# Kernel tuning notes

Hardware: AMD Instinct MI355X
Metric: run time of the kernel (lower is better)

## Reference

```python
import jax, jax.numpy as jnp
import numpy as np

N_EMBD = 2048
EPS = 1e-5

def layernorm(x, g, b):
    mu = jnp.mean(x, axis=-1, keepdims=True)
    var = jnp.mean(jnp.square(x - mu), axis=-1, keepdims=True)
    return (x - mu) * jax.lax.rsqrt(var + EPS) * g + b

def gelu_erf(x):
    return x * 0.5 * (1.0 + jax.lax.erf(x / jnp.sqrt(jnp.asarray(2.0, x.dtype))))

def setup_inputs() -> dict:
    key = jax.random.key(0)
    ks = jax.random.split(key, 2)
    x = jax.random.normal(ks[0], (4, 4096, N_EMBD), dtype=jnp.float32)
    W = jax.random.normal(ks[1], (N_EMBD, N_EMBD), dtype=jnp.float32) / np.sqrt(N_EMBD)
    bW = jnp.zeros((N_EMBD,), jnp.float32)
    g1 = jnp.ones((N_EMBD,), jnp.float32)
    b1 = jnp.zeros((N_EMBD,), jnp.float32)
    g2 = jnp.ones((N_EMBD,), jnp.float32)
    b2 = jnp.zeros((N_EMBD,), jnp.float32)
    return {"x": x, "W": W, "bW": bW, "g1": g1, "b1": b1, "g2": g2, "b2": b2}

def reference(x, W, bW, g1, b1, g2, b2):
    h = layernorm(x, g1, b1)                         # [B,S,D]
    h = jnp.einsum('bsd,ed->bse', h, W) + bW         # Linear(D,D)
    h = gelu_erf(h)
    return layernorm(h, g2, b2)
```

## Files before the change

kernel.cpp:

```cpp
#include <hip/hip_runtime.h>
#include <hip/hip_bf16.h>
#include <math.h>


#define D 2048
#define MROWS 16384
#define BMT 256
#define BNT 256
#define NS 64

typedef __bf16 bf16x8 __attribute__((ext_vector_type(8)));
typedef float f32x4 __attribute__((ext_vector_type(4)));

#define GLP(p) ((const __attribute__((address_space(1))) void*)(p))
#define LDSP(p) ((__attribute__((address_space(3))) void*)(p))
#define S_VMCNT(n) asm volatile("s_waitcnt vmcnt(" #n ")" ::: "memory")
#define MEMFENCE() asm volatile("" ::: "memory")
#define BAR() __builtin_amdgcn_s_barrier()
#define SCHED_FENCE() __builtin_amdgcn_sched_barrier(0)

__device__ __forceinline__ float gelu_f(float v) {
  return 0.5f * v * (1.0f + erff(v * 0.70710678118654752f));
}

__global__ __launch_bounds__(256) void ln1_kernel(
    const float* __restrict__ x, const float* __restrict__ g,
    const float* __restrict__ b, __hip_bfloat16* __restrict__ out) {
  const int tid = threadIdx.x;
  const size_t row = blockIdx.x;
  const float4* xr = (const float4*)(x + row * D);
  float4 v0 = xr[2 * tid];
  float4 v1 = xr[2 * tid + 1];
  float s  = v0.x + v0.y + v0.z + v0.w + v1.x + v1.y + v1.z + v1.w;
  float ss = v0.x*v0.x + v0.y*v0.y + v0.z*v0.z + v0.w*v0.w
           + v1.x*v1.x + v1.y*v1.y + v1.z*v1.z + v1.w*v1.w;
#pragma unroll
  for (int off = 32; off > 0; off >>= 1) {
    s  += __shfl_down(s, off, 64);
    ss += __shfl_down(ss, off, 64);
  }
  __shared__ float red[8];
  const int w = tid >> 6;
  if ((tid & 63) == 0) { red[w] = s; red[w + 4] = ss; }
  __syncthreads();
  s  = red[0] + red[1] + red[2] + red[3];
  ss = red[4] + red[5] + red[6] + red[7];
  const float mu  = s * (1.0f / D);
  const float var = ss * (1.0f / D) - mu * mu;
  const float inv = rsqrtf(var + 1e-5f);
  const float4* gv = (const float4*)g;
  const float4* bv = (const float4*)b;
  float4 g0 = gv[2 * tid], g1 = gv[2 * tid + 1];
  float4 b0 = bv[2 * tid], b1 = bv[2 * tid + 1];
  alignas(16) __hip_bfloat16 h[8];
  h[0] = __float2bfloat16((v0.x - mu) * inv * g0.x + b0.x);
  h[1] = __float2bfloat16((v0.y - mu) * inv * g0.y + b0.y);
  h[2] = __float2bfloat16((v0.z - mu) * inv * g0.z + b0.z);
  h[3] = __float2bfloat16((v0.w - mu) * inv * g0.w + b0.w);
  h[4] = __float2bfloat16((v1.x - mu) * inv * g1.x + b1.x);
  h[5] = __float2bfloat16((v1.y - mu) * inv * g1.y + b1.y);
  h[6] = __float2bfloat16((v1.z - mu) * inv * g1.z + b1.z);
  h[7] = __float2bfloat16((v1.w - mu) * inv * g1.w + b1.w);
  *(uint4*)(out + row * D + (size_t)tid * 8) = *(const uint4*)h;
}

__global__ __launch_bounds__(256) void cvt_kernel(
    const float* __restrict__ W, __hip_bfloat16* __restrict__ Wb, int n8) {
  const int i = blockIdx.x * 256 + threadIdx.x;
  if (i >= n8) return;
  const float4* p = (const float4*)W + 2 * (size_t)i;
  float4 a = p[0], c = p[1];
  alignas(16) __hip_bfloat16 h[8] = {
      __float2bfloat16(a.x), __float2bfloat16(a.y),
      __float2bfloat16(a.z), __float2bfloat16(a.w),
      __float2bfloat16(c.x), __float2bfloat16(c.y),
      __float2bfloat16(c.z), __float2bfloat16(c.w)};
  *(uint4*)(Wb + (size_t)i * 8) = *(const uint4*)h;
}

__global__ __launch_bounds__(512, 2) void gemm_kernel(
    const __hip_bfloat16* __restrict__ A,
    const __hip_bfloat16* __restrict__ Bw,
    const float* __restrict__ bias,
    float* __restrict__ C) {
  __shared__ __hip_bfloat16 sA[4 * 8192];
  __shared__ __hip_bfloat16 sB[4 * 8192];
  const int tid = threadIdx.x;
  const int l = tid & 63;
  const int wid = tid >> 6;
  const int fr = l & 15;
  const int lk = l >> 4;
  const size_t m0 = (size_t)blockIdx.x * BMT;
  const int n0 = blockIdx.y * BNT;
  const int whm = wid >> 2;
  const int wn = (wid & 3) * 64;

  const int srow = ((tid >> 6) << 4) + (tid & 15);
  const int scol = ((tid >> 4) & 3) * 8;
  const int ldd = tid * 16;
  const __hip_bfloat16* const Ag = A + m0 * D + (size_t)srow * D + scol;
  const __hip_bfloat16* const Bg = Bw + (size_t)n0 * D + (size_t)srow * D + scol;

  auto stgA = [&](int s) {
    const int ro = (s & 3) << 14;
    __builtin_amdgcn_global_load_lds(GLP(Ag + s * 32), LDSP((char*)sA + ro + ldd), 16, 0, 0);
    __builtin_amdgcn_global_load_lds(GLP(Ag + (size_t)128 * D + s * 32), LDSP((char*)sA + ro + 8192 + ldd), 16, 0, 0);
  };
  auto stgB = [&](int s) {
    const int ro = (s & 3) << 14;
    __builtin_amdgcn_global_load_lds(GLP(Bg + s * 32), LDSP((char*)sB + ro + ldd), 16, 0, 0);
    __builtin_amdgcn_global_load_lds(GLP(Bg + (size_t)128 * D + s * 32), LDSP((char*)sB + ro + 8192 + ldd), 16, 0, 0);
  };

  bf16x8 a[8], b[4];
  f32x4 acc[8][4] = {};
  const int abase = whm * 8192 + l * 16;
  const int bbase = (wid & 3) * 4096 + l * 16;

  auto rdA8 = [&](int s) {
    const char* pa = (const char*)sA + ((s & 3) << 14) + abase;
#pragma unroll
    for (int mi = 0; mi < 8; ++mi) a[mi] = *(const bf16x8*)(pa + mi * 1024);
  };
  auto rdB2 = [&](int s, int half) {
    const char* pb = (const char*)sB + ((s & 3) << 14) + bbase;
    b[half * 2]     = *(const bf16x8*)(pb + (half * 2) * 1024);
    b[half * 2 + 1] = *(const bf16x8*)(pb + (half * 2 + 1) * 1024);
  };
  auto mma16 = [&](int half) {
    __builtin_amdgcn_s_setprio(1);
#pragma unroll
    for (int mi = 0; mi < 8; ++mi)
#pragma unroll
      for (int jb = 0; jb < 2; ++jb) {
        const int ni = half * 2 + jb;
        acc[mi][ni] = __builtin_amdgcn_mfma_f32_16x16x32_bf16(a[mi], b[ni], acc[mi][ni], 0, 0, 0);
      }
    __builtin_amdgcn_s_setprio(0);
  };

  stgA(0); stgB(0); stgA(1); stgB(1); stgA(2); stgB(2);
  S_VMCNT(8);
  BAR(); MEMFENCE(); SCHED_FENCE();

  for (int s = 0; s < NS; ++s) {
    rdA8(s); rdB2(s, 0);
    if (s < 61) stgA(s + 3);
    BAR();
    mma16(0);
    BAR();
    rdB2(s, 1);
    if (s < 61) stgB(s + 3);
    BAR();
    mma16(1);
    if (s < 61) { S_VMCNT(8); }
    else if (s == 61) { S_VMCNT(4); }
    else if (s == 62) { S_VMCNT(0); }
    BAR(); MEMFENCE(); SCHED_FENCE();
  }

  float bv[4];
#pragma unroll
  for (int ni = 0; ni < 4; ++ni) bv[ni] = bias[n0 + wn + ni * 16 + fr];
#pragma unroll
  for (int mi = 0; mi < 8; ++mi) {
    const size_t rbase = m0 + whm * 128 + mi * 16 + lk * 4;
#pragma unroll
    for (int rr = 0; rr < 4; ++rr) {
      float* crow = C + (rbase + rr) * D + n0 + wn + fr;
#pragma unroll
      for (int ni = 0; ni < 4; ++ni)
        crow[ni * 16] = gelu_f(acc[mi][ni][rr] + bv[ni]);
    }
  }
}

__global__ __launch_bounds__(256) void ln2_kernel(
    float* __restrict__ C, const float* __restrict__ g, const float* __restrict__ b) {
  const int tid = threadIdx.x;
  const size_t row = blockIdx.x;
  float4* cr = (float4*)(C + row * D);
  float4 v0 = cr[2 * tid], v1 = cr[2 * tid + 1];
  float s  = v0.x + v0.y + v0.z + v0.w + v1.x + v1.y + v1.z + v1.w;
  float ss = v0.x*v0.x + v0.y*v0.y + v0.z*v0.z + v0.w*v0.w
           + v1.x*v1.x + v1.y*v1.y + v1.z*v1.z + v1.w*v1.w;
#pragma unroll
  for (int off = 32; off > 0; off >>= 1) {
    s  += __shfl_down(s, off, 64);
    ss += __shfl_down(ss, off, 64);
  }
  __shared__ float red[8];
  const int w = tid >> 6;
  if ((tid & 63) == 0) { red[w] = s; red[w + 4] = ss; }
  __syncthreads();
  s  = red[0] + red[1] + red[2] + red[3];
  ss = red[4] + red[5] + red[6] + red[7];
  const float mu  = s * (1.0f / D);
  const float var = ss * (1.0f / D) - mu * mu;
  const float inv = rsqrtf(var + 1e-5f);
  const float4* gv = (const float4*)g;
  const float4* bv = (const float4*)b;
  float4 g0 = gv[2 * tid], g1 = gv[2 * tid + 1];
  float4 b0 = bv[2 * tid], b1 = bv[2 * tid + 1];
  float4 o0, o1;
  o0.x = (v0.x - mu) * inv * g0.x + b0.x;
  o0.y = (v0.y - mu) * inv * g0.y + b0.y;
  o0.z = (v0.z - mu) * inv * g0.z + b0.z;
  o0.w = (v0.w - mu) * inv * g0.w + b0.w;
  o1.x = (v1.x - mu) * inv * g1.x + b1.x;
  o1.y = (v1.y - mu) * inv * g1.y + b1.y;
  o1.z = (v1.z - mu) * inv * g1.z + b1.z;
  o1.w = (v1.w - mu) * inv * g1.w + b1.w;
  cr[2 * tid] = o0;
  cr[2 * tid + 1] = o1;
}

extern "C" void kernel_launch(void* const* d_in, const int* in_sizes, int n_in,
                              void* d_out, int out_size, void* d_ws, size_t ws_size,
                              hipStream_t stream) {
  const float* x  = (const float*)d_in[0];
  const float* W  = (const float*)d_in[1];
  const float* bW = (const float*)d_in[2];
  const float* g1 = (const float*)d_in[3];
  const float* b1 = (const float*)d_in[4];
  const float* g2 = (const float*)d_in[5];
  const float* b2 = (const float*)d_in[6];
  float* out = (float*)d_out;

  __hip_bfloat16* Abf = (__hip_bfloat16*)d_ws;
  __hip_bfloat16* Wbf = Abf + (size_t)MROWS * D;

  ln1_kernel<<<MROWS, 256, 0, stream>>>(x, g1, b1, Abf);
  cvt_kernel<<<(D * D / 8) / 256, 256, 0, stream>>>(W, Wbf, D * D / 8);
  dim3 grid(MROWS / BMT, D / BNT);
  gemm_kernel<<<grid, 512, 0, stream>>>(Abf, Wbf, bW, out);
  ln2_kernel<<<MROWS, 256, 0, stream>>>(out, g2, b2);
}
```

Before: 258.3 us.

## Double-buffer LDS fragment registers to overlap LDS reads with MFMA in GEMM

Restructures the GEMM main loop into a ping-pong schedule. Each K-step's A and B fragments are read from LDS into one register set while MFMAs run on the other set. The step count drops from four to one barrier per K-step, and the global-to-LDS prefetches for both operands are issued together. Doubling the fragment registers (another 12 bf16x8 vectors) raises VGPR pressure under launch_bounds(512,2) and could cause spills or lower occupancy. The ring is 4 stages with 3-ahead prefetch, so the LDS-slot reuse margin is tight.

```diff
diff --git a/kernel.cpp b/kernel.cpp
--- a/kernel.cpp
+++ b/kernel.cpp
@@ -112,52 +112,65 @@
     __builtin_amdgcn_global_load_lds(GLP(Bg + (size_t)128 * D + s * 32), LDSP((char*)sB + ro + 8192 + ldd), 16, 0, 0);
   };
 
-  bf16x8 a[8], b[4];
-  f32x4 acc[8][4] = {};
   const int abase = whm * 8192 + l * 16;
   const int bbase = (wid & 3) * 4096 + l * 16;
 
-  auto rdA8 = [&](int s) {
+  bf16x8 aE[8], bE[4], aO[8], bO[4];
+  f32x4 acc[8][4] = {};
+
+  auto rdA = [&](int s, bf16x8* ar) {
     const char* pa = (const char*)sA + ((s & 3) << 14) + abase;
 #pragma unroll
-    for (int mi = 0; mi < 8; ++mi) a[mi] = *(const bf16x8*)(pa + mi * 1024);
-  };
-  auto rdB2 = [&](int s, int half) {
+    for (int mi = 0; mi < 8; ++mi) ar[mi] = *(const bf16x8*)(pa + mi * 1024);
+  };
+  auto rdB = [&](int s, bf16x8* br) {
     const char* pb = (const char*)sB + ((s & 3) << 14) + bbase;
-    b[half * 2]     = *(const bf16x8*)(pb + (half * 2) * 1024);
-    b[half * 2 + 1] = *(const bf16x8*)(pb + (half * 2 + 1) * 1024);
-  };
-  auto mma16 = [&](int half) {
+#pragma unroll
+    for (int ni = 0; ni < 4; ++ni) br[ni] = *(const bf16x8*)(pb + ni * 1024);
+  };
+  auto mma32 = [&](const bf16x8* ar, const bf16x8* br) {
     __builtin_amdgcn_s_setprio(1);
 #pragma unroll
     for (int mi = 0; mi < 8; ++mi)
 #pragma unroll
-      for (int jb = 0; jb < 2; ++jb) {
-        const int ni = half * 2 + jb;
-        acc[mi][ni] = __builtin_amdgcn_mfma_f32_16x16x32_bf16(a[mi], b[ni], acc[mi][ni], 0, 0, 0);
-      }
+      for (int ni = 0; ni < 4; ++ni)
+        acc[mi][ni] = __builtin_amdgcn_mfma_f32_16x16x32_bf16(ar[mi], br[ni], acc[mi][ni], 0, 0, 0);
     __builtin_amdgcn_s_setprio(0);
   };
 
   stgA(0); stgB(0); stgA(1); stgB(1); stgA(2); stgB(2);
   S_VMCNT(8);
   BAR(); MEMFENCE(); SCHED_FENCE();
-
-  for (int s = 0; s < NS; ++s) {
-    rdA8(s); rdB2(s, 0);
-    if (s < 61) stgA(s + 3);
-    BAR();
-    mma16(0);
-    BAR();
-    rdB2(s, 1);
-    if (s < 61) stgB(s + 3);
-    BAR();
-    mma16(1);
-    if (s < 61) { S_VMCNT(8); }
-    else if (s == 61) { S_VMCNT(4); }
-    else if (s == 62) { S_VMCNT(0); }
+  rdA(0, aE); rdB(0, bE);
+  S_VMCNT(4);
+  BAR(); MEMFENCE(); SCHED_FENCE();
+
+  for (int sp = 0; sp < 30; ++sp) {
+    const int s0 = 2 * sp;
+    rdA(s0 + 1, aO); rdB(s0 + 1, bO);
+    stgA(s0 + 3); stgB(s0 + 3);
+    mma32(aE, bE);
+    S_VMCNT(4);
     BAR(); MEMFENCE(); SCHED_FENCE();
-  }
+    rdA(s0 + 2, aE); rdB(s0 + 2, bE);
+    stgA(s0 + 4); stgB(s0 + 4);
+    mma32(aO, bO);
+    S_VMCNT(4);
+    BAR(); MEMFENCE(); SCHED_FENCE();
+  }
+  rdA(61, aO); rdB(61, bO);
+  stgA(63); stgB(63);
+  mma32(aE, bE);
+  S_VMCNT(4);
+  BAR(); MEMFENCE(); SCHED_FENCE();
+  rdA(62, aE); rdB(62, bE);
+  mma32(aO, bO);
+  S_VMCNT(0);
+  BAR(); MEMFENCE(); SCHED_FENCE();
+  rdA(63, aO); rdB(63, bO);
+  mma32(aE, bE);
+  BAR(); MEMFENCE(); SCHED_FENCE();
+  mma32(aO, bO);
 
   float bv[4];
 #pragma unroll
```

Result: faster. 248.7 us (-3.7%).

## Simplify GEMM pipeline to one barrier per stage and swizzle blocks per XCD

Applied to the files above, without the earlier changes.

The GEMM main loop moves from four barriers and two half-step MFMA phases per K-stage to a single wait-and-barrier at the top of each stage. Each stage now reads all A and B fragments, issues the prefetch for stage s+3 into the slot freed in the previous iteration, and runs all 32 MFMAs together. The 2D grid becomes a 1D grid with a remap that gives each XCD (nid&7) a contiguous band of M tiles across all N tiles, to improve L2 reuse of A and W. The cost is less interleaving of LDS reads with MFMAs inside a stage, and four B fragments held in registers at once.

```diff
diff --git a/kernel.cpp b/kernel.cpp
--- a/kernel.cpp
+++ b/kernel.cpp
@@ -15,7 +15,6 @@
 #define GLP(p) ((const __attribute__((address_space(1))) void*)(p))
 #define LDSP(p) ((__attribute__((address_space(3))) void*)(p))
 #define S_VMCNT(n) asm volatile("s_waitcnt vmcnt(" #n ")" ::: "memory")
-#define MEMFENCE() asm volatile("" ::: "memory")
 #define BAR() __builtin_amdgcn_s_barrier()
 #define SCHED_FENCE() __builtin_amdgcn_sched_barrier(0)
 
@@ -90,8 +89,14 @@
   const int wid = tid >> 6;
   const int fr = l & 15;
   const int lk = l >> 4;
-  const size_t m0 = (size_t)blockIdx.x * BMT;
-  const int n0 = blockIdx.y * BNT;
+
+  const int nid = blockIdx.x;
+  const int xk = nid & 7, j = nid >> 3;
+  const int bx = (xk << 3) | (j >> 3);
+  const int by = j & 7;
+  const size_t m0 = (size_t)bx * BMT;
+  const int n0 = by * BNT;
+
   const int whm = wid >> 2;
   const int wn = (wid & 3) * 64;
 
@@ -112,51 +117,42 @@
     __builtin_amdgcn_global_load_lds(GLP(Bg + (size_t)128 * D + s * 32), LDSP((char*)sB + ro + 8192 + ldd), 16, 0, 0);
   };
 
+  const int abase = whm * 8192 + l * 16;
+  const int bbase = (wid & 3) * 4096 + l * 16;
+
   bf16x8 a[8], b[4];
   f32x4 acc[8][4] = {};
-  const int abase = whm * 8192 + l * 16;
-  const int bbase = (wid & 3) * 4096 + l * 16;
-
-  auto rdA8 = [&](int s) {
+
+  auto rdA = [&](int s) {
     const char* pa = (const char*)sA + ((s & 3) << 14) + abase;
 #pragma unroll
     for (int mi = 0; mi < 8; ++mi) a[mi] = *(const bf16x8*)(pa + mi * 1024);
   };
-  auto rdB2 = [&](int s, int half) {
+  auto rdB = [&](int s) {
     const char* pb = (const char*)sB + ((s & 3) << 14) + bbase;
-    b[half * 2]     = *(const bf16x8*)(pb + (half * 2) * 1024);
-    b[half * 2 + 1] = *(const bf16x8*)(pb + (half * 2 + 1) * 1024);
-  };
-  auto mma16 = [&](int half) {
+#pragma unroll
+    for (int ni = 0; ni < 4; ++ni) b[ni] = *(const bf16x8*)(pb + ni * 1024);
+  };
+  auto mma32 = [&]() {
     __builtin_amdgcn_s_setprio(1);
 #pragma unroll
     for (int mi = 0; mi < 8; ++mi)
 #pragma unroll
-      for (int jb = 0; jb < 2; ++jb) {
-        const int ni = half * 2 + jb;
+      for (int ni = 0; ni < 4; ++ni)
         acc[mi][ni] = __builtin_amdgcn_mfma_f32_16x16x32_bf16(a[mi], b[ni], acc[mi][ni], 0, 0, 0);
-      }
     __builtin_amdgcn_s_setprio(0);
   };
 
   stgA(0); stgB(0); stgA(1); stgB(1); stgA(2); stgB(2);
-  S_VMCNT(8);
-  BAR(); MEMFENCE(); SCHED_FENCE();
 
   for (int s = 0; s < NS; ++s) {
-    rdA8(s); rdB2(s, 0);
-    if (s < 61) stgA(s + 3);
-    BAR();
-    mma16(0);
-    BAR();
-    rdB2(s, 1);
-    if (s < 61) stgB(s + 3);
-    BAR();
-    mma16(1);
-    if (s < 61) { S_VMCNT(8); }
-    else if (s == 61) { S_VMCNT(4); }
-    else if (s == 62) { S_VMCNT(0); }
-    BAR(); MEMFENCE(); SCHED_FENCE();
+    if (s <= 61) { S_VMCNT(8); }
+    else if (s == 62) { S_VMCNT(4); }
+    else { S_VMCNT(0); }
+    BAR(); SCHED_FENCE();
+    rdA(s); rdB(s);
+    if (s < 61) { stgA(s + 3); stgB(s + 3); }
+    mma32();
   }
 
   float bv[4];
@@ -232,7 +228,6 @@
 
   ln1_kernel<<<MROWS, 256, 0, stream>>>(x, g1, b1, Abf);
   cvt_kernel<<<(D * D / 8) / 256, 256, 0, stream>>>(W, Wbf, D * D / 8);
-  dim3 grid(MROWS / BMT, D / BNT);
-  gemm_kernel<<<grid, 512, 0, stream>>>(Abf, Wbf, bW, out);
+  gemm_kernel<<<(MROWS / BMT) * (D / BNT), 512, 0, stream>>>(Abf, Wbf, bW, out);
   ln2_kernel<<<MROWS, 256, 0, stream>>>(out, g2, b2);
 }
```

Result: faster. 246.6 us (-4.5%).
